# Performance work log

Measured on AMD Instinct MI355X. Metric: run time of the kernel, lower is better.

Reference implementation:

```python
import jax, jax.numpy as jnp
import numpy as np

STRIDES = (4, 8, 16, 32)   # featmap_strides (FPN levels)
TAU = 2.0                  # level-weight temperature (translate_to_linear_weight)
G = 4                      # n_groups
SP = 32                    # spatial_points
TP = 8                     # temporal_points == T frames
D = 256                    # query_dim == feat_channels
CG = D // G                # channels per group
EFF = CG                   # eff_in_dim == eff_out_dim in AdaptiveMixing
OUT_S = SP * 4             # out_points (spatial), out_multiplier = 4
OUT_T = TP * 4
B, Q, T, IMG = 4, 100, 8, 256


def _ln2(x, eps=1e-5):
    # F.layer_norm over the last TWO dims, no affine params
    mu = jnp.mean(x, axis=(-2, -1), keepdims=True)
    var = jnp.var(x, axis=(-2, -1), keepdims=True)
    return (x - mu) * jax.lax.rsqrt(var + eps)


def _ln(x, g, b, eps=1e-5):
    mu = jnp.mean(x, axis=-1, keepdims=True)
    var = jnp.var(x, axis=-1, keepdims=True)
    return (x - mu) * jax.lax.rsqrt(var + eps) * g + b


def _bilinear(feat, px, py):
    # feat: [B,H,W,T,G,Cg]; px,py: [B,Q,G,S] pixel coords
    # grid_sample semantics: bilinear, align_corners=False, zero padding
    Bn, H, W, Tn, Gn, Cg = feat.shape
    bidx = jnp.arange(Bn)[:, None, None, None]
    gidx = jnp.arange(Gn)[None, None, :, None]
    x0 = jnp.floor(px); y0 = jnp.floor(py)
    fx = px - x0; fy = py - y0
    x0i = x0.astype(jnp.int32); y0i = y0.astype(jnp.int32)
    out = 0.0
    for dx, dy, w in ((0, 0, (1 - fx) * (1 - fy)), (1, 0, fx * (1 - fy)),
                      (0, 1, (1 - fx) * fy), (1, 1, fx * fy)):
        xi = x0i + dx; yi = y0i + dy
        valid = (xi >= 0) & (xi < W) & (yi >= 0) & (yi < H)
        xc = jnp.clip(xi, 0, W - 1); yc = jnp.clip(yi, 0, H - 1)
        v = feat[bidx, yc, xc, :, gidx, :]   # [B,Q,G,S,T,Cg]
        out = out + v * (w * valid)[..., None, None]
    return out


def _adaptive_mixing(x, query, Wp, bp, Wo, bo, n_in, n_out):
    # x: [B,Q,G,P,Cg]; per-instance dynamic channel mixing then point mixing
    Bn, Qn = x.shape[:2]
    params = (query @ Wp + bp).reshape(Bn, Qn, G, -1)
    M = params[..., :EFF * EFF].reshape(Bn, Qn, G, EFF, EFF)
    S = params[..., EFF * EFF:].reshape(Bn, Qn, G, n_out, n_in)
    out = jnp.einsum('bqgpc,bqgcd->bqgpd', x, M)
    out = jax.nn.relu(_ln2(out))
    out = jnp.einsum('bqgop,bqgpd->bqgod', S, out)
    out = jax.nn.relu(_ln2(out))
    out = out.reshape(Bn, Qn, -1) @ Wo + bo
    return query + out


def _forward(feat0, feat1, feat2, feat3, proposal_boxes, spatial_queries, temporal_queries,
             W_off, b_off, W_ps, b_ps, Wo_s, bo_s, g_s, be_s,
             W_pt, b_pt, Wo_t, bo_t, g_t, be_t):
    feats = (feat0, feat1, feat2, feat3)
    Bn, Qn, _ = spatial_queries.shape
    # offset_generator + make_sample_points (xyzr proposal boxes)
    off = (spatial_queries @ W_off + b_off).reshape(Bn, Qn, G * SP, 3)
    cc = proposal_boxes[..., None, :2]
    scale = 2.0 ** proposal_boxes[..., None, 2:3]
    r = proposal_boxes[..., None, 3:4]
    wh = scale * jnp.concatenate([2.0 ** (-0.5 * r), 2.0 ** (0.5 * r)], axis=-1)
    xy = (cc + off[..., :2] * wh).reshape(Bn, Qn, G, SP, 2)
    z = (proposal_boxes[..., None, 2] + off[..., 2]).reshape(Bn, Qn, G, SP)
    # soft level weights over log2-scale distance (translate_to_linear_weight)
    mapped = z - jnp.float32(float(np.log2(STRIDES[0])))
    lvls = jnp.arange(len(STRIDES), dtype=z.dtype)
    lw = jax.nn.softmax(-((mapped[..., None] - lvls) ** 2) / TAU, axis=-1)
    sampled = 0.0
    for i, feat in enumerate(feats):
        Bc, C, Tn, H, W = feat.shape
        fr = feat.transpose(0, 3, 4, 2, 1).reshape(Bc, H, W, Tn, G, CG)
        px = xy[..., 0] / STRIDES[i] - 0.5
        py = xy[..., 1] / STRIDES[i] - 0.5
        sampled = sampled + _bilinear(fr, px, py) * lw[..., i][..., None, None]
    sampled = sampled.transpose(0, 1, 2, 4, 3, 5)     # [B,Q,G,T,SP,Cg]
    spatial_feats = jnp.mean(sampled, axis=3)         # mean over T   -> [B,Q,G,SP,Cg]
    temporal_feats = jnp.mean(sampled, axis=4)        # mean over SP  -> [B,Q,G,T,Cg]
    sq = _adaptive_mixing(spatial_feats, spatial_queries, W_ps, b_ps, Wo_s, bo_s, SP, OUT_S)
    sq = _ln(sq, g_s, be_s)
    tq = _adaptive_mixing(temporal_feats, temporal_queries, W_pt, b_pt, Wo_t, bo_t, TP, OUT_T)
    tq = _ln(tq, g_t, be_t)
    return sq, tq


def setup_inputs() -> dict:
    key = jax.random.key(0)
    ks = jax.random.split(key, 24)
    f32 = jnp.float32
    inp = {}
    for i, s in enumerate(STRIDES):
        h = IMG // s
        inp['feat%d' % i] = jax.random.normal(ks[i], (B, D, T, h, h), dtype=f32)
    # xyzr boxes: center xy in image coords, z = log2 box scale, r = log2 aspect
    inp['proposal_boxes'] = jnp.concatenate([
        jax.random.uniform(ks[4], (B, Q, 2), dtype=f32) * IMG,
        jax.random.uniform(ks[5], (B, Q, 1), dtype=f32) * 3.0 + 3.0,
        jax.random.normal(ks[6], (B, Q, 1), dtype=f32) * 0.25,
    ], axis=-1)
    PS = EFF * EFF + SP * OUT_S
    PT = EFF * EFF + TP * OUT_T
    inp.update(
        spatial_queries=jax.random.normal(ks[7], (B, Q, D), dtype=f32),
        temporal_queries=jax.random.normal(ks[8], (B, Q, D), dtype=f32),
        W_off=jax.random.normal(ks[9], (D, SP * G * 3), dtype=f32) * 0.01,
        b_off=jax.random.normal(ks[10], (SP * G * 3,), dtype=f32) * 0.1,
        W_ps=jax.random.normal(ks[11], (D, G * PS), dtype=f32) * 0.02,
        b_ps=jax.random.normal(ks[12], (G * PS,), dtype=f32) * 0.02,
        Wo_s=jax.random.normal(ks[13], (G * EFF * OUT_S, D), dtype=f32) * 0.02,
        bo_s=jax.random.normal(ks[14], (D,), dtype=f32) * 0.02,
        g_s=jnp.ones((D,), dtype=f32),
        be_s=jnp.zeros((D,), dtype=f32),
        W_pt=jax.random.normal(ks[15], (D, G * PT), dtype=f32) * 0.02,
        b_pt=jax.random.normal(ks[16], (G * PT,), dtype=f32) * 0.02,
        Wo_t=jax.random.normal(ks[17], (G * EFF * OUT_T, D), dtype=f32) * 0.02,
        bo_t=jax.random.normal(ks[18], (D,), dtype=f32) * 0.02,
        g_t=jnp.ones((D,), dtype=f32),
        be_t=jnp.zeros((D,), dtype=f32),
    )
    return inp


def reference(feat0, feat1, feat2, feat3, proposal_boxes, spatial_queries, temporal_queries,
              W_off, b_off, W_ps, b_ps, Wo_s, bo_s, g_s, be_s,
              W_pt, b_pt, Wo_t, bo_t, g_t, be_t):
    return _forward(feat0, feat1, feat2, feat3, proposal_boxes, spatial_queries, temporal_queries,
                    W_off, b_off, W_ps, b_ps, Wo_s, bo_s, g_s, be_s,
                    W_pt, b_pt, Wo_t, bo_t, g_t, be_t)
```

## Files before the change

### kernel.cpp

```cpp
#include <hip/hip_runtime.h>
#include <hip/hip_bf16.h>


typedef __attribute__((ext_vector_type(8))) short bf16x8;
typedef __attribute__((ext_vector_type(8))) unsigned short u16x8;
typedef __attribute__((ext_vector_type(4))) float f32x4;

static __device__ __forceinline__ unsigned short f2bf(float f){
  unsigned u = __float_as_uint(f);
  u += 0x7fffu + ((u >> 16) & 1u);
  return (unsigned short)(u >> 16);
}
static __device__ __forceinline__ float bf2f(unsigned short h){
  return __uint_as_float(((unsigned)h) << 16);
}

__global__ __launch_bounds__(256) void k_wtrans_all(
    const float* __restrict__ Wps, const float* __restrict__ Wpt,
    const float* __restrict__ Wos, const float* __restrict__ Wot,
    unsigned short* __restrict__ WpsP, unsigned short* __restrict__ WptP,
    unsigned short* __restrict__ WosP, unsigned short* __restrict__ WotP,
    const float4* __restrict__ qs, const float4* __restrict__ qt,
    unsigned short* __restrict__ qsP, unsigned short* __restrict__ qtP){
  int id = blockIdx.x;
  if(id >= 5696){
    int blk = id - 5696;
    const float4* in; unsigned short* out; int i;
    if(blk < 100){ in = qs; out = qsP; i = blk*256 + threadIdx.x; }
    else         { in = qt; out = qtP; i = (blk-100)*256 + threadIdx.x; }
    float4 v = in[i];
    int row = i >> 6, k0 = (i & 63) * 4;
    int strip = row >> 4, colr = row & 15;
    int kk = k0 >> 5, kg = (k0 >> 3) & 3, e0 = k0 & 7;
    size_t dst = ((size_t)(strip*8 + kk)*64 + kg*16 + colr)*8 + e0;
    *(ushort4*)(out + dst) = make_ushort4(f2bf(v.x), f2bf(v.y), f2bf(v.z), f2bf(v.w));
    return;
  }
  const float* in; unsigned short* out; int N, KKtot, r0, c0;
  if(id < 2048){       in=Wps; out=WpsP; N=32768; KKtot=8;    c0=(id>>2)*64;        r0=(id&3)*64; }
  else if(id < 3136){ int i=id-2048; in=Wpt; out=WptP; N=17408; KKtot=8;    c0=(i>>2)*64; r0=(i&3)*64; }
  else if(id < 5184){ int i=id-3136; in=Wos; out=WosP; N=256;   KKtot=1024; c0=(i&3)*64;  r0=(i>>2)*64; }
  else {              int i=id-5184; in=Wot; out=WotP; N=256;   KKtot=256;  c0=(i&3)*64;  r0=(i>>2)*64; }
  __shared__ float tile[64][65];
  int lane = threadIdx.x & 63, wid = threadIdx.x >> 6;
  #pragma unroll
  for(int i=0;i<16;i++){
    int r = wid + 4*i;
    tile[r][lane] = in[(size_t)(r0 + r) * N + c0 + lane];
  }
  __syncthreads();
  int t = threadIdx.x;
  int ch = t >> 5, w2 = t & 31;
  int kk_l = ch >> 2, st_l = ch & 3;
  size_t chunkbase = ((size_t)((c0>>4) + st_l) * KKtot + ((r0>>5) + kk_l)) * 512;
  #pragma unroll
  for(int j=0;j<2;j++){
    int pl = w2*2 + j;
    int kg = pl >> 4, cc = pl & 15;
    u16x8 v;
    #pragma unroll
    for(int e=0;e<8;e++) v[e] = f2bf(tile[kk_l*32 + kg*8 + e][st_l*16 + cc]);
    *(u16x8*)(out + chunkbase + pl*8) = v;
  }
}

__global__ __launch_bounds__(384) void k_offsets(
    const float* __restrict__ q, const float* __restrict__ Woff,
    const float* __restrict__ boff, const float* __restrict__ boxes,
    float* __restrict__ xybuf, float* __restrict__ lwbuf){
  int bq = blockIdx.x;
  __shared__ float qsh[256];
  __shared__ float off[384];
  int tid = threadIdx.x;
  if(tid < 256) qsh[tid] = q[bq*256 + tid];
  __syncthreads();
  float acc = boff[tid];
  for(int k=0;k<256;k++) acc = fmaf(qsh[k], Woff[k*384 + tid], acc);
  off[tid] = acc;
  __syncthreads();
  if(tid < 128){
    float cx = boxes[bq*4+0], cy = boxes[bq*4+1];
    float zb = boxes[bq*4+2], r  = boxes[bq*4+3];
    float wx = exp2f(zb - 0.5f*r);
    float wy = exp2f(zb + 0.5f*r);
    float x = cx + off[tid*3+0]*wx;
    float y = cy + off[tid*3+1]*wy;
    float z = zb + off[tid*3+2];
    xybuf[(bq*128+tid)*2+0] = x;
    xybuf[(bq*128+tid)*2+1] = y;
    float m = z - 2.0f;
    float e0 = -0.5f*(m-0.f)*(m-0.f);
    float e1 = -0.5f*(m-1.f)*(m-1.f);
    float e2 = -0.5f*(m-2.f)*(m-2.f);
    float e3 = -0.5f*(m-3.f)*(m-3.f);
    float mx = fmaxf(fmaxf(e0,e1), fmaxf(e2,e3));
    float s0 = expf(e0-mx), s1 = expf(e1-mx), s2 = expf(e2-mx), s3 = expf(e3-mx);
    float inv = 1.0f/(s0+s1+s2+s3);
    lwbuf[(bq*128+tid)*4+0] = s0*inv;
    lwbuf[(bq*128+tid)*4+1] = s1*inv;
    lwbuf[(bq*128+tid)*4+2] = s2*inv;
    lwbuf[(bq*128+tid)*4+3] = s3*inv;
  }
}

__global__ __launch_bounds__(256) void k_feat_transpose_all(
    const float* __restrict__ f0, const float* __restrict__ f1,
    const float* __restrict__ f2, const float* __restrict__ f3,
    unsigned short* __restrict__ o0, unsigned short* __restrict__ o1,
    unsigned short* __restrict__ o2, unsigned short* __restrict__ o3){
  int px = blockIdx.x;
  const float* in; unsigned short* out; int P, p0;
  if(px < 64){      in=f0; out=o0; P=4096; p0=px*64; }
  else if(px < 80){ in=f1; out=o1; P=1024; p0=(px-64)*64; }
  else if(px < 84){ in=f2; out=o2; P=256;  p0=(px-80)*64; }
  else {            in=f3; out=o3; P=64;   p0=0; }
  __shared__ float tile[64][65];
  int c0 = blockIdx.y * 64;
  int b = blockIdx.z >> 3, t = blockIdx.z & 7;
  int lane = threadIdx.x & 63, wid = threadIdx.x >> 6;
  size_t inbase = ((size_t)b * 2048 + t) * (size_t)P;
  #pragma unroll
  for(int i=0;i<16;i++){
    int c = wid + 4*i;
    tile[c][lane] = in[inbase + (size_t)(c0 + c) * 8 * P + p0 + lane];
  }
  __syncthreads();
  size_t outbase = (size_t)b * P * 2048 + (size_t)t * 256;
  #pragma unroll
  for(int i=0;i<16;i++){
    int p = wid + 4*i;
    out[outbase + (size_t)(p0 + p) * 2048 + c0 + lane] = f2bf(tile[lane][p]);
  }
}

__global__ __launch_bounds__(256, 4) void k_sample(
    const unsigned short* __restrict__ f0, const unsigned short* __restrict__ f1,
    const unsigned short* __restrict__ f2, const unsigned short* __restrict__ f3,
    const float* __restrict__ xybuf, const float* __restrict__ lwbuf,
    float* __restrict__ sfeat, float* __restrict__ tfeat){
  int bid = blockIdx.x;
  int g = bid & 3, bq = bid >> 2;
  int b = bq / 100;
  __shared__ unsigned smp[32][8][32];
  __shared__ int   soff[128][4];
  __shared__ float swt [128][4];
  int tid = threadIdx.x;
  if(tid < 128){
    int sp = tid >> 2, l = tid & 3;
    float x  = xybuf[(bq*128 + g*32 + sp)*2+0];
    float y  = xybuf[(bq*128 + g*32 + sp)*2+1];
    float lw = lwbuf[(bq*128 + g*32 + sp)*4 + l];
    float inv = (l==0) ? 0.25f : (l==1) ? 0.125f : (l==2) ? 0.0625f : 0.03125f;
    int W = 64 >> l;
    float px = x*inv - 0.5f, py = y*inv - 0.5f;
    float x0f = floorf(px), y0f = floorf(py);
    int x0 = (int)x0f, y0 = (int)y0f;
    float fx = px - x0f, fy = py - y0f;
    #pragma unroll
    for(int tap=0; tap<4; tap++){
      int dx = tap & 1, dy = tap >> 1;
      int xi = x0 + dx, yi = y0 + dy;
      bool valid = (xi >= 0) & (xi < W) & (yi >= 0) & (yi < W);
      int xc = min(max(xi, 0), W-1), yc = min(max(yi, 0), W-1);
      float w = (dx ? fx : 1.f-fx) * (dy ? fy : 1.f-fy) * lw;
      soff[tid][tap] = (yc*W + xc) * 4096;
      swt [tid][tap] = valid ? w : 0.f;
    }
  }
  __syncthreads();
  int cp = tid & 31, t = tid >> 5;
  int tcb = t*256 + g*64 + cp*2;
  const char* fb0 = (const char*)(f0 + (size_t)b*4096*2048 + tcb);
  const char* fb1 = (const char*)(f1 + (size_t)b*1024*2048 + tcb);
  const char* fb2 = (const char*)(f2 + (size_t)b* 256*2048 + tcb);
  const char* fb3 = (const char*)(f3 + (size_t)b*  64*2048 + tcb);
  float t0 = 0.f, t1 = 0.f;
  #pragma unroll 2
  for(int sp=0; sp<32; sp++){
    float a0 = 0.f, a1 = 0.f;
    #pragma unroll
    for(int l=0; l<4; l++){
      int idx = sp*4 + l;
      const char* fb = (l==0) ? fb0 : (l==1) ? fb1 : (l==2) ? fb2 : fb3;
      #pragma unroll
      for(int tap=0; tap<4; tap++){
        int off = soff[idx][tap];
        float w = swt[idx][tap];
        unsigned v = *(const unsigned*)(fb + (size_t)off);
        a0 = fmaf(w, __uint_as_float((v & 0xffffu) << 16), a0);
        a1 = fmaf(w, __uint_as_float(v & 0xffff0000u),      a1);
      }
    }
    smp[sp][t][cp] = (unsigned)f2bf(a0) | ((unsigned)f2bf(a1) << 16);
    t0 += a0; t1 += a1;
  }
  __syncthreads();
  {
    size_t o = ((size_t)(bq*4 + g)*8 + t)*64 + cp*2;
    tfeat[o+0] = t0 * (1.f/32.f);
    tfeat[o+1] = t1 * (1.f/32.f);
  }
  #pragma unroll
  for(int i=0;i<4;i++){
    int j = tid + 256*i;
    int sp = j >> 5, p = j & 31;
    float s0 = 0.f, s1 = 0.f;
    #pragma unroll
    for(int tt=0; tt<8; tt++){
      unsigned v = smp[sp][tt][p];
      s0 += __uint_as_float((v & 0xffffu) << 16);
      s1 += __uint_as_float(v & 0xffff0000u);
    }
    size_t o = ((size_t)(bq*4 + g)*32 + sp)*64 + p*2;
    sfeat[o+0] = s0 * 0.125f;
    sfeat[o+1] = s1 * 0.125f;
  }
}

__global__ __launch_bounds__(256, 4) void k_gemm_params(
    const unsigned short* __restrict__ As, const unsigned short* __restrict__ WTs,
    const float* __restrict__ biass, unsigned short* __restrict__ outs,
    const unsigned short* __restrict__ At, const unsigned short* __restrict__ WTt,
    const float* __restrict__ biast, unsigned short* __restrict__ outt){
  const unsigned short *A, *W; const float* bias; unsigned short* out; int N, nb;
  if(blockIdx.x < 512){ A=As; W=WTs; bias=biass; out=outs; N=32768; nb=blockIdx.x; }
  else                { A=At; W=WTt; bias=biast; out=outt; N=17408; nb=blockIdx.x-512; }
  int wave = threadIdx.x >> 6, lane = threadIdx.x & 63;
  int strip = nb*4 + wave;
  int col = lane & 15, kg = lane >> 4;
  const bf16x8* wp = (const bf16x8*)W + (size_t)strip*8*64 + lane;
  bf16x8 bfrag[8];
  #pragma unroll
  for(int k=0;k<8;k++) bfrag[k] = wp[k*64];
  float bv = bias[strip*16 + col];
  int mt0 = blockIdx.y * 5;
  #pragma unroll
  for(int m=0; m<5; m++){
    int mt = mt0 + m;
    f32x4 acc = {bv, bv, bv, bv};
    const bf16x8* ap = (const bf16x8*)A + (size_t)mt*8*64 + lane;
    bf16x8 af[8];
    #pragma unroll
    for(int k=0;k<8;k++) af[k] = ap[k*64];
    #pragma unroll
    for(int k=0;k<8;k++)
      acc = __builtin_amdgcn_mfma_f32_16x16x32_bf16(af[k], bfrag[k], acc, 0, 0, 0);
    int rowb = mt*16 + kg*4;
    #pragma unroll
    for(int r=0;r<4;r++)
      out[(size_t)(rowb + r) * N + strip*16 + col] = f2bf(acc[r]);
  }
}

static __device__ __forceinline__ void block_reduce2(
    float& s1, float& s2, float* rA, float* rB, int tid){
  #pragma unroll
  for(int o=32;o;o>>=1){ s1 += __shfl_xor(s1,o); s2 += __shfl_xor(s2,o); }
  int wave = tid >> 6, lane = tid & 63;
  if(lane == 0){ rA[wave] = s1; rB[wave] = s2; }
  __syncthreads();
  s1 = rA[0]+rA[1]+rA[2]+rA[3];
  s2 = rB[0]+rB[1]+rB[2]+rB[3];
}

template<int P, int O>
__global__ __launch_bounds__(256) void k_mix(
    const float* __restrict__ feats, const unsigned short* __restrict__ params,
    unsigned short* __restrict__ hidden, int KK){
  int bid = blockIdx.x; int g = bid & 3, bq = bid >> 2;
  const int PG = 4096 + O*P;
  const unsigned short* pp = params + (size_t)bq * 4 * PG + (size_t)g * PG;
  const float* xin = feats + (size_t)(bq*4 + g) * P * 64;
  __shared__ float xs[P][64];
  __shared__ float o1[P][64];
  __shared__ float Ss[O*P];
  __shared__ float rA[4], rB[4];
  int tid = threadIdx.x; int d = tid & 63; int pb = tid >> 6;
  for(int i=tid; i<P*64; i+=256) xs[i>>6][i&63] = xin[i];
  for(int i=tid; i<O*P; i+=256) Ss[i] = bf2f(pp[4096 + i]);
  __syncthreads();
  constexpr int NP = P/4;
  float a[NP];
  #pragma unroll
  for(int i=0;i<NP;i++) a[i] = 0.f;
  for(int c=0;c<64;c++){
    float mv = bf2f(pp[c*64 + d]);
    #pragma unroll
    for(int i=0;i<NP;i++) a[i] = fmaf(xs[pb + 4*i][c], mv, a[i]);
  }
  float s1 = 0.f, s2 = 0.f;
  #pragma unroll
  for(int i=0;i<NP;i++){ s1 += a[i]; s2 += a[i]*a[i]; }
  block_reduce2(s1, s2, rA, rB, tid);
  {
    const float n = (float)(P*64);
    float mu = s1/n, var = s2/n - mu*mu;
    float rstd = rsqrtf(var + 1e-5f);
    #pragma unroll
    for(int i=0;i<NP;i++){
      float v = (a[i] - mu) * rstd;
      o1[pb + 4*i][d] = fmaxf(v, 0.f);
    }
  }
  __syncthreads();
  constexpr int NO = O/4;
  float bacc[NO];
  #pragma unroll
  for(int i=0;i<NO;i++){
    float acc = 0.f;
    int o = pb + 4*i;
    #pragma unroll
    for(int p=0;p<P;p++) acc = fmaf(Ss[o*P + p], o1[p][d], acc);
    bacc[i] = acc;
  }
  s1 = 0.f; s2 = 0.f;
  #pragma unroll
  for(int i=0;i<NO;i++){ s1 += bacc[i]; s2 += bacc[i]*bacc[i]; }
  block_reduce2(s1, s2, rA, rB, tid);
  {
    const float n = (float)(O*64);
    float mu = s1/n, var = s2/n - mu*mu;
    float rstd = rsqrtf(var + 1e-5f);
    int strip = bq >> 4, colr = bq & 15;
    int kg = (d >> 3) & 3, e = d & 7, dh = d >> 5;
    #pragma unroll
    for(int i=0;i<NO;i++){
      int o = pb + 4*i;
      float v = (bacc[i] - mu) * rstd;
      int kk = (g*O + o)*2 + dh;
      size_t addr = ((size_t)(strip*KK + kk)*64 + kg*16 + colr)*8 + e;
      hidden[addr] = f2bf(fmaxf(v, 0.f));
    }
  }
}

__global__ __launch_bounds__(256, 4) void k_gemm_final(
    const unsigned short* __restrict__ Hs, const unsigned short* __restrict__ WTs,
    float* __restrict__ parts, const unsigned short* __restrict__ Ht,
    const unsigned short* __restrict__ WTt, float* __restrict__ partt){
  const unsigned short *H, *W; float* partial; int KK, ks, ksteps;
  if(blockIdx.x < 64){ H=Hs; W=WTs; partial=parts; KK=1024; ks=blockIdx.x;    ksteps=16; }
  else               { H=Ht; W=WTt; partial=partt; KK=256;  ks=blockIdx.x-64; ksteps=4;  }
  int wave = threadIdx.x >> 6, lane = threadIdx.x & 63;
  int col = lane & 15, kg = lane >> 4;
  int mt = blockIdx.y;
  int kk0 = ks * ksteps;
  int n0 = wave * 64;
  f32x4 acc[4] = {};
  const bf16x8* ap  = (const bf16x8*)H + ((size_t)mt*KK + kk0)*64 + lane;
  const bf16x8* bp0 = (const bf16x8*)W + ((size_t)(4*wave+0)*KK + kk0)*64 + lane;
  const bf16x8* bp1 = (const bf16x8*)W + ((size_t)(4*wave+1)*KK + kk0)*64 + lane;
  const bf16x8* bp2 = (const bf16x8*)W + ((size_t)(4*wave+2)*KK + kk0)*64 + lane;
  const bf16x8* bp3 = (const bf16x8*)W + ((size_t)(4*wave+3)*KK + kk0)*64 + lane;
  #pragma unroll 4
  for(int kk=0; kk<ksteps; kk++){
    bf16x8 af = ap[kk*64];
    bf16x8 b0 = bp0[kk*64], b1 = bp1[kk*64], b2 = bp2[kk*64], b3 = bp3[kk*64];
    acc[0] = __builtin_amdgcn_mfma_f32_16x16x32_bf16(af, b0, acc[0], 0,0,0);
    acc[1] = __builtin_amdgcn_mfma_f32_16x16x32_bf16(af, b1, acc[1], 0,0,0);
    acc[2] = __builtin_amdgcn_mfma_f32_16x16x32_bf16(af, b2, acc[2], 0,0,0);
    acc[3] = __builtin_amdgcn_mfma_f32_16x16x32_bf16(af, b3, acc[3], 0,0,0);
  }
  int rowb = mt*16 + kg*4;
  #pragma unroll
  for(int nt=0; nt<4; nt++)
    #pragma unroll
    for(int r=0; r<4; r++)
      partial[((size_t)ks*400 + rowb + r)*256 + n0 + nt*16 + col] = acc[nt][r];
}

template<int NS>
__global__ __launch_bounds__(256) void k_finalize(
    const float* __restrict__ part_s, const float* __restrict__ part_t,
    const float* __restrict__ qs, const float* __restrict__ qt,
    const float* __restrict__ bos, const float* __restrict__ bot,
    const float* __restrict__ gs, const float* __restrict__ gt,
    const float* __restrict__ bes, const float* __restrict__ bet,
    float* __restrict__ out_s, float* __restrict__ out_t){
  __shared__ float rA[4], rB[4];
  int bq = blockIdx.x, j = threadIdx.x;
  const float *partial, *q, *bo, *gam, *bet_;
  float* out;
  if(blockIdx.y == 0){ partial=part_s; q=qs; bo=bos; gam=gs; bet_=bes; out=out_s; }
  else               { partial=part_t; q=qt; bo=bot; gam=gt; bet_=bet; out=out_t; }
  float v = q[bq*256 + j] + bo[j];
  #pragma unroll 8
  for(int s=0;s<NS;s++) v += partial[((size_t)s*400 + bq)*256 + j];
  float s1 = v, s2 = v*v;
  block_reduce2(s1, s2, rA, rB, j);
  float mu = s1 * (1.f/256.f);
  float var = s2 * (1.f/256.f) - mu*mu;
  float rstd = rsqrtf(var + 1e-5f);
  out[bq*256 + j] = (v - mu) * rstd * gam[j] + bet_[j];
}

extern "C" void kernel_launch(void* const* d_in, const int* in_sizes, int n_in,
                              void* d_out, int out_size, void* d_ws, size_t ws_size,
                              hipStream_t stream){
  const float* feat0 = (const float*)d_in[0];
  const float* feat1 = (const float*)d_in[1];
  const float* feat2 = (const float*)d_in[2];
  const float* feat3 = (const float*)d_in[3];
  const float* boxes = (const float*)d_in[4];
  const float* qs    = (const float*)d_in[5];
  const float* qt    = (const float*)d_in[6];
  const float* Woff  = (const float*)d_in[7];
  const float* boff  = (const float*)d_in[8];
  const float* Wps   = (const float*)d_in[9];
  const float* bps   = (const float*)d_in[10];
  const float* Wos   = (const float*)d_in[11];
  const float* bos   = (const float*)d_in[12];
  const float* gs    = (const float*)d_in[13];
  const float* bes   = (const float*)d_in[14];
  const float* Wpt   = (const float*)d_in[15];
  const float* bpt   = (const float*)d_in[16];
  const float* Wot   = (const float*)d_in[17];
  const float* bot   = (const float*)d_in[18];
  const float* gt    = (const float*)d_in[19];
  const float* bet   = (const float*)d_in[20];

  char* ws = (char*)d_ws;
  unsigned short* featT0 = (unsigned short*)(ws + 0);
  unsigned short* featT1 = (unsigned short*)(ws + 67108864);
  unsigned short* featT2 = (unsigned short*)(ws + 83886080);
  unsigned short* featT3 = (unsigned short*)(ws + 88080384);
  unsigned short* params_s = (unsigned short*)(ws + 0);
  unsigned short* params_t = (unsigned short*)(ws + 52428800);
  float* part_s          = (float*)(ws + 0);
  float* part_t          = (float*)(ws + 52428800);
  unsigned short* qsP    = (unsigned short*)(ws + 89128960);
  unsigned short* qtP    = (unsigned short*)(ws + 89333760);
  unsigned short* WpsP   = (unsigned short*)(ws + 89538560);
  unsigned short* WptP   = (unsigned short*)(ws + 106315776);
  unsigned short* WosP   = (unsigned short*)(ws + 115228672);
  unsigned short* WotP   = (unsigned short*)(ws + 132005888);
  float* xybuf           = (float*)(ws + 136232960);
  float* lwbuf           = (float*)(ws + 136642560);
  float* sfeat           = (float*)(ws + 137461760);
  float* tfeat           = (float*)(ws + 150568960);
  unsigned short* hid_s  = (unsigned short*)(ws + 153845760);
  unsigned short* hid_t  = (unsigned short*)(ws + 180060160);
  float* out_s = (float*)d_out;
  float* out_t = out_s + 102400;

  k_wtrans_all<<<5896, 256, 0, stream>>>(Wps, Wpt, Wos, Wot, WpsP, WptP, WosP, WotP,
                                         (const float4*)qs, (const float4*)qt, qsP, qtP);
  k_feat_transpose_all<<<dim3(85, 4, 32), 256, 0, stream>>>(
      feat0, feat1, feat2, feat3, featT0, featT1, featT2, featT3);
  k_offsets<<<400, 384, 0, stream>>>(qs, Woff, boff, boxes, xybuf, lwbuf);
  k_sample<<<1600, 256, 0, stream>>>(featT0, featT1, featT2, featT3,
                                     xybuf, lwbuf, sfeat, tfeat);
  k_gemm_params<<<dim3(784, 5), 256, 0, stream>>>(qsP, WpsP, bps, params_s,
                                                  qtP, WptP, bpt, params_t);
  k_mix<32,128><<<1600, 256, 0, stream>>>(sfeat, params_s, hid_s, 1024);
  k_mix< 8, 32><<<1600, 256, 0, stream>>>(tfeat, params_t, hid_t, 256);
  k_gemm_final<<<dim3(128, 25), 256, 0, stream>>>(hid_s, WosP, part_s,
                                                  hid_t, WotP, part_t);
  k_finalize<64><<<dim3(400, 2), 256, 0, stream>>>(
      part_s, part_t, qs, qt, bos, bot, gs, gt, bes, bet, out_s, out_t);
}
```

Baseline: 287.1 us.

## Merge sampling and param GEMM into one launch, vectorize feature transpose

Fuses the bilinear sampling kernel and the dynamic-parameter GEMM into a single launch, with extra blocks dispatched by block index. The two independent stages can then run at the same time and one launch boundary goes away. Because params previously aliased the transposed feature buffer that sampling reads, params now get their own workspace region to avoid a race. The feature transpose also switches to float4 loads and ushort4 stores, which may raise LDS bank conflicts on the column reads.

```diff
diff --git a/kernel.cpp b/kernel.cpp
--- a/kernel.cpp
+++ b/kernel.cpp
@@ -117,27 +117,71 @@
   __shared__ float tile[64][65];
   int c0 = blockIdx.y * 64;
   int b = blockIdx.z >> 3, t = blockIdx.z & 7;
-  int lane = threadIdx.x & 63, wid = threadIdx.x >> 6;
+  int tid = threadIdx.x;
   size_t inbase = ((size_t)b * 2048 + t) * (size_t)P;
   #pragma unroll
-  for(int i=0;i<16;i++){
-    int c = wid + 4*i;
-    tile[c][lane] = in[inbase + (size_t)(c0 + c) * 8 * P + p0 + lane];
+  for(int j=0;j<4;j++){
+    int idx = j*256 + tid;
+    int c = idx >> 4, q4 = idx & 15;
+    float4 v = *(const float4*)(in + inbase + (size_t)(c0 + c) * 8 * P + p0 + q4*4);
+    tile[c][q4*4+0] = v.x; tile[c][q4*4+1] = v.y;
+    tile[c][q4*4+2] = v.z; tile[c][q4*4+3] = v.w;
   }
   __syncthreads();
   size_t outbase = (size_t)b * P * 2048 + (size_t)t * 256;
   #pragma unroll
-  for(int i=0;i<16;i++){
-    int p = wid + 4*i;
-    out[outbase + (size_t)(p0 + p) * 2048 + c0 + lane] = f2bf(tile[lane][p]);
-  }
-}
-
-__global__ __launch_bounds__(256, 4) void k_sample(
+  for(int j=0;j<4;j++){
+    int idx = j*256 + tid;
+    int p = idx >> 4, q4 = idx & 15;
+    ushort4 o;
+    o.x = f2bf(tile[q4*4+0][p]); o.y = f2bf(tile[q4*4+1][p]);
+    o.z = f2bf(tile[q4*4+2][p]); o.w = f2bf(tile[q4*4+3][p]);
+    *(ushort4*)(out + outbase + (size_t)(p0 + p) * 2048 + c0 + q4*4) = o;
+  }
+}
+
+__global__ __launch_bounds__(256, 4) void k_sample_params(
     const unsigned short* __restrict__ f0, const unsigned short* __restrict__ f1,
     const unsigned short* __restrict__ f2, const unsigned short* __restrict__ f3,
     const float* __restrict__ xybuf, const float* __restrict__ lwbuf,
-    float* __restrict__ sfeat, float* __restrict__ tfeat){
+    float* __restrict__ sfeat, float* __restrict__ tfeat,
+    const unsigned short* __restrict__ As, const unsigned short* __restrict__ WTs,
+    const float* __restrict__ biass, unsigned short* __restrict__ outs,
+    const unsigned short* __restrict__ At, const unsigned short* __restrict__ WTt,
+    const float* __restrict__ biast, unsigned short* __restrict__ outt){
+  if(blockIdx.x >= 1600){
+    int flat = blockIdx.x - 1600;
+    int nb = flat % 784, my = flat / 784;
+    const unsigned short *A, *W; const float* bias; unsigned short* out; int N, nbl;
+    if(nb < 512){ A=As; W=WTs; bias=biass; out=outs; N=32768; nbl=nb; }
+    else        { A=At; W=WTt; bias=biast; out=outt; N=17408; nbl=nb-512; }
+    int wave = threadIdx.x >> 6, lane = threadIdx.x & 63;
+    int strip = nbl*4 + wave;
+    int col = lane & 15, kg = lane >> 4;
+    const bf16x8* wp = (const bf16x8*)W + (size_t)strip*8*64 + lane;
+    bf16x8 bfrag[8];
+    #pragma unroll
+    for(int k=0;k<8;k++) bfrag[k] = wp[k*64];
+    float bv = bias[strip*16 + col];
+    int mt0 = my * 5;
+    #pragma unroll
+    for(int m=0; m<5; m++){
+      int mt = mt0 + m;
+      f32x4 acc = {bv, bv, bv, bv};
+      const bf16x8* ap = (const bf16x8*)A + (size_t)mt*8*64 + lane;
+      bf16x8 af[8];
+      #pragma unroll
+      for(int k=0;k<8;k++) af[k] = ap[k*64];
+      #pragma unroll
+      for(int k=0;k<8;k++)
+        acc = __builtin_amdgcn_mfma_f32_16x16x32_bf16(af[k], bfrag[k], acc, 0, 0, 0);
+      int rowb = mt*16 + kg*4;
+      #pragma unroll
+      for(int r=0;r<4;r++)
+        out[(size_t)(rowb + r) * N + strip*16 + col] = f2bf(acc[r]);
+    }
+    return;
+  }
   int bid = blockIdx.x;
   int g = bid & 3, bq = bid >> 2;
   int b = bq / 100;
@@ -214,41 +258,6 @@
     size_t o = ((size_t)(bq*4 + g)*32 + sp)*64 + p*2;
     sfeat[o+0] = s0 * 0.125f;
     sfeat[o+1] = s1 * 0.125f;
-  }
-}
-
-__global__ __launch_bounds__(256, 4) void k_gemm_params(
-    const unsigned short* __restrict__ As, const unsigned short* __restrict__ WTs,
-    const float* __restrict__ biass, unsigned short* __restrict__ outs,
-    const unsigned short* __restrict__ At, const unsigned short* __restrict__ WTt,
-    const float* __restrict__ biast, unsigned short* __restrict__ outt){
-  const unsigned short *A, *W; const float* bias; unsigned short* out; int N, nb;
-  if(blockIdx.x < 512){ A=As; W=WTs; bias=biass; out=outs; N=32768; nb=blockIdx.x; }
-  else                { A=At; W=WTt; bias=biast; out=outt; N=17408; nb=blockIdx.x-512; }
-  int wave = threadIdx.x >> 6, lane = threadIdx.x & 63;
-  int strip = nb*4 + wave;
-  int col = lane & 15, kg = lane >> 4;
-  const bf16x8* wp = (const bf16x8*)W + (size_t)strip*8*64 + lane;
-  bf16x8 bfrag[8];
-  #pragma unroll
-  for(int k=0;k<8;k++) bfrag[k] = wp[k*64];
-  float bv = bias[strip*16 + col];
-  int mt0 = blockIdx.y * 5;
-  #pragma unroll
-  for(int m=0; m<5; m++){
-    int mt = mt0 + m;
-    f32x4 acc = {bv, bv, bv, bv};
-    const bf16x8* ap = (const bf16x8*)A + (size_t)mt*8*64 + lane;
-    bf16x8 af[8];
-    #pragma unroll
-    for(int k=0;k<8;k++) af[k] = ap[k*64];
-    #pragma unroll
-    for(int k=0;k<8;k++)
-      acc = __builtin_amdgcn_mfma_f32_16x16x32_bf16(af[k], bfrag[k], acc, 0, 0, 0);
-    int rowb = mt*16 + kg*4;
-    #pragma unroll
-    for(int r=0;r<4;r++)
-      out[(size_t)(rowb + r) * N + strip*16 + col] = f2bf(acc[r]);
   }
 }
 
@@ -424,8 +433,6 @@
   unsigned short* featT1 = (unsigned short*)(ws + 67108864);
   unsigned short* featT2 = (unsigned short*)(ws + 83886080);
   unsigned short* featT3 = (unsigned short*)(ws + 88080384);
-  unsigned short* params_s = (unsigned short*)(ws + 0);
-  unsigned short* params_t = (unsigned short*)(ws + 52428800);
   float* part_s          = (float*)(ws + 0);
   float* part_t          = (float*)(ws + 52428800);
   unsigned short* qsP    = (unsigned short*)(ws + 89128960);
@@ -440,6 +447,8 @@
   float* tfeat           = (float*)(ws + 150568960);
   unsigned short* hid_s  = (unsigned short*)(ws + 153845760);
   unsigned short* hid_t  = (unsigned short*)(ws + 180060160);
+  unsigned short* params_s = (unsigned short*)(ws + 186613760);
+  unsigned short* params_t = (unsigned short*)(ws + 212828160);
   float* out_s = (float*)d_out;
   float* out_t = out_s + 102400;
 
@@ -448,10 +457,10 @@
   k_feat_transpose_all<<<dim3(85, 4, 32), 256, 0, stream>>>(
       feat0, feat1, feat2, feat3, featT0, featT1, featT2, featT3);
   k_offsets<<<400, 384, 0, stream>>>(qs, Woff, boff, boxes, xybuf, lwbuf);
-  k_sample<<<1600, 256, 0, stream>>>(featT0, featT1, featT2, featT3,
-                                     xybuf, lwbuf, sfeat, tfeat);
-  k_gemm_params<<<dim3(784, 5), 256, 0, stream>>>(qsP, WpsP, bps, params_s,
-                                                  qtP, WptP, bpt, params_t);
+  k_sample_params<<<5520, 256, 0, stream>>>(featT0, featT1, featT2, featT3,
+                                            xybuf, lwbuf, sfeat, tfeat,
+                                            qsP, WpsP, bps, params_s,
+                                            qtP, WptP, bpt, params_t);
   k_mix<32,128><<<1600, 256, 0, stream>>>(sfeat, params_s, hid_s, 1024);
   k_mix< 8, 32><<<1600, 256, 0, stream>>>(tfeat, params_t, hid_t, 256);
   k_gemm_final<<<dim3(128, 25), 256, 0, stream>>>(hid_s, WosP, part_s,
```

Measured after the change: 279.3 us. 1.03x faster.
